# Performance work log

Hardware: AMD Instinct MI355X
Metric: run time of the kernel (lower is better)

The kernel has to match this reference:

```python
import jax, jax.numpy as jnp
import numpy as np

S = 0.7071067811865476  # 1/sqrt(2), pywt haar filter coefficient
# For output j=2k the source coord is k-0.25 (frac 0.75), for j=2k+1 it is k+0.25 (frac 0.25).
_WE = (-0.03515625, 0.26171875, 0.87890625, -0.10546875)  # even outputs, taps at k-2..k+1


def haar_dwt2(x):
    # pywt wavedec2 single level with 'haar': cA=(x0+x1)/sqrt2, cD=(x0-x1)/sqrt2 per pair
    a = (x[..., ::2] + x[..., 1::2]) * S
    d = (x[..., ::2] - x[..., 1::2]) * S
    aa = (a[..., ::2, :] + a[..., 1::2, :]) * S   # LL
    da = (a[..., ::2, :] - a[..., 1::2, :]) * S   # cH (LH)
    ad = (d[..., ::2, :] + d[..., 1::2, :]) * S   # cV (HL)
    dd = (d[..., ::2, :] - d[..., 1::2, :]) * S   # cD (HH)
    return aa, da, ad, dd


def _interleave(e, o, axis):
    stacked = jnp.stack([e, o], axis=axis)
    shp = list(e.shape)
    shp[axis] *= 2
    return stacked.reshape(shp)


def haar_idwt2(aa, da, ad, dd):
    # invert columns (axis -2): x0=(a+d)/sqrt2, x1=(a-d)/sqrt2
    a = _interleave((aa + da) * S, (aa - da) * S, -2)
    d = _interleave((ad + dd) * S, (ad - dd) * S, -2)
    return _interleave((a + d) * S, (a - d) * S, -1)


def area_down2(x):
    h, w = x.shape[-2] // 2, x.shape[-1] // 2
    return x.reshape(*x.shape[:-2], h, 2, w, 2).mean(axis=(-3, -1))


def _up2_last(x):
    n = x.shape[-1]
    p = jnp.pad(x, [(0, 0)] * (x.ndim - 1) + [(2, 2)], mode='edge')  # replicate border like cv2
    ev = (_WE[0] * p[..., 0:n] + _WE[1] * p[..., 1:n + 1]
          + _WE[2] * p[..., 2:n + 2] + _WE[3] * p[..., 3:n + 3])
    od = (_WE[3] * p[..., 1:n + 1] + _WE[2] * p[..., 2:n + 2]
          + _WE[1] * p[..., 3:n + 3] + _WE[0] * p[..., 4:n + 4])
    return jnp.stack([ev, od], axis=-1).reshape(*x.shape[:-1], 2 * n)


def cubic_up2(x):
    x = _up2_last(x)
    return jnp.swapaxes(_up2_last(jnp.swapaxes(x, -1, -2)), -1, -2)


def dwt_roundtrip(x):
    B, C, H, W = x.shape
    # ---- encode ----
    aa1, lh1, hl1, hh1 = haar_dwt2(x)          # level 1: [B,C,H/2,W/2]
    ll2, lh2, hl2, hh2 = haar_dwt2(aa1)        # level 2: [B,C,H/4,W/4]
    bands = jnp.stack([ll2, lh2, hl2, hh2,
                       area_down2(lh1), area_down2(hl1), area_down2(hh1)], axis=2)
    z = bands.reshape(B, C * 7, H // 4, W // 4)
    # ---- decode ----
    b = z.reshape(B, C, 7, H // 4, W // 4)
    lh1u = cubic_up2(b[:, :, 4])
    hl1u = cubic_up2(b[:, :, 5])
    hh1u = cubic_up2(b[:, :, 6])
    aa1r = haar_idwt2(b[:, :, 0], b[:, :, 1], b[:, :, 2], b[:, :, 3])
    return haar_idwt2(aa1r, lh1u, hl1u, hh1u)


def setup_inputs() -> dict:
    key = jax.random.key(0)
    x = jax.random.normal(key, (32, 3, 512, 512), dtype=jnp.float32)
    return {"x": x}


def reference(x):
    return dwt_roundtrip(x)
```

## Files before the change

kernel.cpp:

```cpp
#include <hip/hip_runtime.h>


#define WE0 (-0.03515625f)
#define WE1 (0.26171875f)
#define WE2 (0.87890625f)
#define WE3 (-0.10546875f)

__global__ __launch_bounds__(256) void dwt_encode_kernel(
    const float* __restrict__ x,
    float* __restrict__ aa1,
    float* __restrict__ dlh,
    float* __restrict__ dhl,
    float* __restrict__ dhh)
{
    const int t  = blockIdx.x * 256 + threadIdx.x;
    const int c4 = t & 127;
    const int r4 = (t >> 7) & 127;
    const int bc = t >> 14;

    const float* xp = x + ((size_t)bc << 18);

    float v[4][4];
#pragma unroll
    for (int i = 0; i < 4; ++i) {
        const float4 rv = *reinterpret_cast<const float4*>(
            xp + (size_t)(4 * r4 + i) * 512 + 4 * c4);
        v[i][0] = rv.x; v[i][1] = rv.y; v[i][2] = rv.z; v[i][3] = rv.w;
    }

    float aa[2][2], lhs = 0.f, hls = 0.f, hhs = 0.f;
#pragma unroll
    for (int sr = 0; sr < 2; ++sr) {
#pragma unroll
        for (int sc = 0; sc < 2; ++sc) {
            const float x00 = v[2 * sr][2 * sc],     x01 = v[2 * sr][2 * sc + 1];
            const float x10 = v[2 * sr + 1][2 * sc], x11 = v[2 * sr + 1][2 * sc + 1];
            aa[sr][sc] = 0.5f * (x00 + x01 + x10 + x11);
            lhs += 0.5f * (x00 + x01 - x10 - x11);
            hls += 0.5f * (x00 - x01 + x10 - x11);
            hhs += 0.5f * (x00 - x01 - x10 + x11);
        }
    }

    float* aap = aa1 + ((size_t)bc << 16);
#pragma unroll
    for (int sr = 0; sr < 2; ++sr) {
        *reinterpret_cast<float2*>(aap + (size_t)(2 * r4 + sr) * 256 + 2 * c4) =
            make_float2(aa[sr][0], aa[sr][1]);
    }

    const size_t di = ((size_t)bc << 14) + ((size_t)r4 << 7) + (size_t)c4;
    dlh[di] = 0.25f * lhs;
    dhl[di] = 0.25f * hls;
    dhh[di] = 0.25f * hhs;
}

__global__ __launch_bounds__(256) void dwt_decode_kernel(
    const float* __restrict__ aa1,
    const float* __restrict__ dlh,
    const float* __restrict__ dhl,
    const float* __restrict__ dhh,
    float* __restrict__ out)
{
    const int t  = blockIdx.x * 256 + threadIdx.x;
    const int kc = t & 127;
    const int kr = (t >> 7) & 127;
    const int bc = t >> 14;

    int rs[5], cs[5];
#pragma unroll
    for (int i = 0; i < 5; ++i) {
        rs[i] = min(max(kr - 2 + i, 0), 127);
        cs[i] = min(max(kc - 2 + i, 0), 127);
    }

    const size_t dbase = ((size_t)bc << 14);
    const float* dp[3] = { dlh + dbase, dhl + dbase, dhh + dbase };

    float U[3][2][2];
#pragma unroll
    for (int b = 0; b < 3; ++b) {
        float he[5], ho[5];
#pragma unroll
        for (int i = 0; i < 5; ++i) {
            const float* row = dp[b] + ((size_t)rs[i] << 7);
            const float d0 = row[cs[0]], d1 = row[cs[1]], d2 = row[cs[2]];
            const float d3 = row[cs[3]], d4 = row[cs[4]];
            he[i] = WE0 * d0 + WE1 * d1 + WE2 * d2 + WE3 * d3;
            ho[i] = WE3 * d1 + WE2 * d2 + WE1 * d3 + WE0 * d4;
        }
        U[b][0][0] = WE0 * he[0] + WE1 * he[1] + WE2 * he[2] + WE3 * he[3];
        U[b][0][1] = WE0 * ho[0] + WE1 * ho[1] + WE2 * ho[2] + WE3 * ho[3];
        U[b][1][0] = WE3 * he[1] + WE2 * he[2] + WE1 * he[3] + WE0 * he[4];
        U[b][1][1] = WE3 * ho[1] + WE2 * ho[2] + WE1 * ho[3] + WE0 * ho[4];
    }

    const float* aap = aa1 + ((size_t)bc << 16);
    float* op = out + ((size_t)bc << 18);

#pragma unroll
    for (int i = 0; i < 2; ++i) {
        const float2 aav = *reinterpret_cast<const float2*>(
            aap + (size_t)(2 * kr + i) * 256 + 2 * kc);
        float o0[4], o1[4];
#pragma unroll
        for (int j = 0; j < 2; ++j) {
            const float aaV = (j == 0) ? aav.x : aav.y;
            const float da = U[0][i][j], ad = U[1][i][j], dd = U[2][i][j];
            const float s1 = aaV + da, dd1 = aaV - da;
            const float s2 = ad + dd,  dd2 = ad - dd;
            o0[2 * j]     = 0.5f * (s1 + s2);
            o0[2 * j + 1] = 0.5f * (s1 - s2);
            o1[2 * j]     = 0.5f * (dd1 + dd2);
            o1[2 * j + 1] = 0.5f * (dd1 - dd2);
        }
        *reinterpret_cast<float4*>(op + (size_t)(4 * kr + 2 * i) * 512 + 4 * kc) =
            make_float4(o0[0], o0[1], o0[2], o0[3]);
        *reinterpret_cast<float4*>(op + (size_t)(4 * kr + 2 * i + 1) * 512 + 4 * kc) =
            make_float4(o1[0], o1[1], o1[2], o1[3]);
    }
}

extern "C" void kernel_launch(void* const* d_in, const int* in_sizes, int n_in,
                              void* d_out, int out_size, void* d_ws, size_t ws_size,
                              hipStream_t stream)
{
    const float* x = (const float*)d_in[0];
    float* out = (float*)d_out;
    float* ws  = (float*)d_ws;

    float* aa1 = ws;
    float* dlh = aa1 + (size_t)96 * 256 * 256;
    float* dhl = dlh + (size_t)96 * 128 * 128;
    float* dhh = dhl + (size_t)96 * 128 * 128;

    const int nthreads = 96 * 128 * 128;
    const int blocks   = nthreads / 256;

    dwt_encode_kernel<<<blocks, 256, 0, stream>>>(x, aa1, dlh, dhl, dhh);
    dwt_decode_kernel<<<blocks, 256, 0, stream>>>(aa1, dlh, dhl, dhh, out);
}
```

Baseline: 192.6 us.

## Fuse encode and decode into one tiled kernel with shared-memory halo bands

Replaces the two-kernel pipeline with a single kernel. Each block handles a 128x128 output tile of one image: it recomputes the level-1 detail bands over a 36x36 haloed region, keeps them and the aa1 tile in LDS, then does the cubic upsample and inverse Haar straight from LDS. This removes the global workspace round trip for aa1 and the detail bands, plus one launch. In exchange the halo input is read redundantly (about 27% extra), only 1536 blocks are launched, and per-block LDS use of roughly 32KB may limit occupancy.

```diff
diff --git a/kernel.cpp b/kernel.cpp
--- a/kernel.cpp
+++ b/kernel.cpp
@@ -6,118 +6,114 @@
 #define WE2 (0.87890625f)
 #define WE3 (-0.10546875f)
 
-__global__ __launch_bounds__(256) void dwt_encode_kernel(
-    const float* __restrict__ x,
-    float* __restrict__ aa1,
-    float* __restrict__ dlh,
-    float* __restrict__ dhl,
-    float* __restrict__ dhh)
+__global__ __launch_bounds__(256) void dwt_fused_kernel(
+    const float* __restrict__ x, float* __restrict__ out)
 {
-    const int t  = blockIdx.x * 256 + threadIdx.x;
-    const int c4 = t & 127;
-    const int r4 = (t >> 7) & 127;
-    const int bc = t >> 14;
+    __shared__ float dband[3][36][36];
+    __shared__ float aaT[64][66];
+
+    const int tid  = threadIdx.x;
+    const int b    = blockIdx.x;
+    const int bc   = b >> 4;
+    const int tile = b & 15;
+    const int tr   = tile >> 2;
+    const int tc   = tile & 3;
 
     const float* xp = x + ((size_t)bc << 18);
+    float* op       = out + ((size_t)bc << 18);
 
-    float v[4][4];
+    const int bdr = tr * 32 - 2;
+    const int bdc = tc * 32 - 2;
+
+    for (int task = tid; task < 36 * 36; task += 256) {
+        const int i = task / 36;
+        const int j = task - 36 * i;
+        const int dr = min(max(bdr + i, 0), 127);
+        const int dc = min(max(bdc + j, 0), 127);
+
+        float v[4][4];
 #pragma unroll
-    for (int i = 0; i < 4; ++i) {
-        const float4 rv = *reinterpret_cast<const float4*>(
-            xp + (size_t)(4 * r4 + i) * 512 + 4 * c4);
-        v[i][0] = rv.x; v[i][1] = rv.y; v[i][2] = rv.z; v[i][3] = rv.w;
-    }
+        for (int r = 0; r < 4; ++r) {
+            const float4 rv = *reinterpret_cast<const float4*>(
+                xp + (size_t)(4 * dr + r) * 512 + 4 * dc);
+            v[r][0] = rv.x; v[r][1] = rv.y; v[r][2] = rv.z; v[r][3] = rv.w;
+        }
 
-    float aa[2][2], lhs = 0.f, hls = 0.f, hhs = 0.f;
+        float aa[2][2];
+        float lhs = 0.f, hls = 0.f, hhs = 0.f;
 #pragma unroll
-    for (int sr = 0; sr < 2; ++sr) {
+        for (int sr = 0; sr < 2; ++sr) {
 #pragma unroll
-        for (int sc = 0; sc < 2; ++sc) {
-            const float x00 = v[2 * sr][2 * sc],     x01 = v[2 * sr][2 * sc + 1];
-            const float x10 = v[2 * sr + 1][2 * sc], x11 = v[2 * sr + 1][2 * sc + 1];
-            aa[sr][sc] = 0.5f * (x00 + x01 + x10 + x11);
-            lhs += 0.5f * (x00 + x01 - x10 - x11);
-            hls += 0.5f * (x00 - x01 + x10 - x11);
-            hhs += 0.5f * (x00 - x01 - x10 + x11);
+            for (int sc = 0; sc < 2; ++sc) {
+                const float x00 = v[2*sr][2*sc],   x01 = v[2*sr][2*sc+1];
+                const float x10 = v[2*sr+1][2*sc], x11 = v[2*sr+1][2*sc+1];
+                aa[sr][sc] = 0.5f * (x00 + x01 + x10 + x11);
+                lhs += 0.5f * (x00 + x01 - x10 - x11);
+                hls += 0.5f * (x00 - x01 + x10 - x11);
+                hhs += 0.5f * (x00 - x01 - x10 + x11);
+            }
+        }
+
+        dband[0][i][j] = 0.25f * lhs;
+        dband[1][i][j] = 0.25f * hls;
+        dband[2][i][j] = 0.25f * hhs;
+
+        if ((unsigned)(i - 2) < 32u && (unsigned)(j - 2) < 32u) {
+            const int ar = 2 * (i - 2), ac = 2 * (j - 2);
+            aaT[ar][ac]     = aa[0][0];
+            aaT[ar][ac + 1] = aa[0][1];
+            aaT[ar + 1][ac]     = aa[1][0];
+            aaT[ar + 1][ac + 1] = aa[1][1];
         }
     }
 
-    float* aap = aa1 + ((size_t)bc << 16);
+    __syncthreads();
+
+    for (int blk = tid; blk < 1024; blk += 256) {
+        const int kr = blk >> 5;
+        const int kc = blk & 31;
+
+        float U[3][2][2];
 #pragma unroll
-    for (int sr = 0; sr < 2; ++sr) {
-        *reinterpret_cast<float2*>(aap + (size_t)(2 * r4 + sr) * 256 + 2 * c4) =
-            make_float2(aa[sr][0], aa[sr][1]);
-    }
+        for (int bb = 0; bb < 3; ++bb) {
+            float he[5], ho[5];
+#pragma unroll
+            for (int i = 0; i < 5; ++i) {
+                const float* rowp = &dband[bb][kr + i][kc];
+                const float d0 = rowp[0], d1 = rowp[1], d2 = rowp[2],
+                            d3 = rowp[3], d4 = rowp[4];
+                he[i] = WE0 * d0 + WE1 * d1 + WE2 * d2 + WE3 * d3;
+                ho[i] = WE3 * d1 + WE2 * d2 + WE1 * d3 + WE0 * d4;
+            }
+            U[bb][0][0] = WE0*he[0] + WE1*he[1] + WE2*he[2] + WE3*he[3];
+            U[bb][0][1] = WE0*ho[0] + WE1*ho[1] + WE2*ho[2] + WE3*ho[3];
+            U[bb][1][0] = WE3*he[1] + WE2*he[2] + WE1*he[3] + WE0*he[4];
+            U[bb][1][1] = WE3*ho[1] + WE2*ho[2] + WE1*ho[3] + WE0*ho[4];
+        }
 
-    const size_t di = ((size_t)bc << 14) + ((size_t)r4 << 7) + (size_t)c4;
-    dlh[di] = 0.25f * lhs;
-    dhl[di] = 0.25f * hls;
-    dhh[di] = 0.25f * hhs;
-}
-
-__global__ __launch_bounds__(256) void dwt_decode_kernel(
-    const float* __restrict__ aa1,
-    const float* __restrict__ dlh,
-    const float* __restrict__ dhl,
-    const float* __restrict__ dhh,
-    float* __restrict__ out)
-{
-    const int t  = blockIdx.x * 256 + threadIdx.x;
-    const int kc = t & 127;
-    const int kr = (t >> 7) & 127;
-    const int bc = t >> 14;
-
-    int rs[5], cs[5];
+        const int orow = tr * 128 + 4 * kr;
+        const int ocol = tc * 128 + 4 * kc;
 #pragma unroll
-    for (int i = 0; i < 5; ++i) {
-        rs[i] = min(max(kr - 2 + i, 0), 127);
-        cs[i] = min(max(kc - 2 + i, 0), 127);
-    }
-
-    const size_t dbase = ((size_t)bc << 14);
-    const float* dp[3] = { dlh + dbase, dhl + dbase, dhh + dbase };
-
-    float U[3][2][2];
+        for (int i = 0; i < 2; ++i) {
+            const float a0 = aaT[2*kr + i][2*kc];
+            const float a1 = aaT[2*kr + i][2*kc + 1];
+            float o0[4], o1[4];
 #pragma unroll
-    for (int b = 0; b < 3; ++b) {
-        float he[5], ho[5];
-#pragma unroll
-        for (int i = 0; i < 5; ++i) {
-            const float* row = dp[b] + ((size_t)rs[i] << 7);
-            const float d0 = row[cs[0]], d1 = row[cs[1]], d2 = row[cs[2]];
-            const float d3 = row[cs[3]], d4 = row[cs[4]];
-            he[i] = WE0 * d0 + WE1 * d1 + WE2 * d2 + WE3 * d3;
-            ho[i] = WE3 * d1 + WE2 * d2 + WE1 * d3 + WE0 * d4;
+            for (int j = 0; j < 2; ++j) {
+                const float aaV = (j == 0) ? a0 : a1;
+                const float da = U[0][i][j], ad = U[1][i][j], dd = U[2][i][j];
+                const float s1 = aaV + da, t1 = aaV - da;
+                const float s2 = ad + dd,  t2 = ad - dd;
+                o0[2*j]     = 0.5f * (s1 + s2);
+                o0[2*j + 1] = 0.5f * (s1 - s2);
+                o1[2*j]     = 0.5f * (t1 + t2);
+                o1[2*j + 1] = 0.5f * (t1 - t2);
+            }
+            *reinterpret_cast<float4*>(op + (size_t)(orow + 2*i) * 512 + ocol) =
+                make_float4(o0[0], o0[1], o0[2], o0[3]);
+            *reinterpret_cast<float4*>(op + (size_t)(orow + 2*i + 1) * 512 + ocol) =
+                make_float4(o1[0], o1[1], o1[2], o1[3]);
         }
-        U[b][0][0] = WE0 * he[0] + WE1 * he[1] + WE2 * he[2] + WE3 * he[3];
-        U[b][0][1] = WE0 * ho[0] + WE1 * ho[1] + WE2 * ho[2] + WE3 * ho[3];
-        U[b][1][0] = WE3 * he[1] + WE2 * he[2] + WE1 * he[3] + WE0 * he[4];
-        U[b][1][1] = WE3 * ho[1] + WE2 * ho[2] + WE1 * ho[3] + WE0 * ho[4];
-    }
-
-    const float* aap = aa1 + ((size_t)bc << 16);
-    float* op = out + ((size_t)bc << 18);
-
-#pragma unroll
-    for (int i = 0; i < 2; ++i) {
-        const float2 aav = *reinterpret_cast<const float2*>(
-            aap + (size_t)(2 * kr + i) * 256 + 2 * kc);
-        float o0[4], o1[4];
-#pragma unroll
-        for (int j = 0; j < 2; ++j) {
-            const float aaV = (j == 0) ? aav.x : aav.y;
-            const float da = U[0][i][j], ad = U[1][i][j], dd = U[2][i][j];
-            const float s1 = aaV + da, dd1 = aaV - da;
-            const float s2 = ad + dd,  dd2 = ad - dd;
-            o0[2 * j]     = 0.5f * (s1 + s2);
-            o0[2 * j + 1] = 0.5f * (s1 - s2);
-            o1[2 * j]     = 0.5f * (dd1 + dd2);
-            o1[2 * j + 1] = 0.5f * (dd1 - dd2);
-        }
-        *reinterpret_cast<float4*>(op + (size_t)(4 * kr + 2 * i) * 512 + 4 * kc) =
-            make_float4(o0[0], o0[1], o0[2], o0[3]);
-        *reinterpret_cast<float4*>(op + (size_t)(4 * kr + 2 * i + 1) * 512 + 4 * kc) =
-            make_float4(o1[0], o1[1], o1[2], o1[3]);
     }
 }
 
@@ -127,16 +123,8 @@
 {
     const float* x = (const float*)d_in[0];
     float* out = (float*)d_out;
-    float* ws  = (float*)d_ws;
+    (void)d_ws; (void)ws_size;
 
-    float* aa1 = ws;
-    float* dlh = aa1 + (size_t)96 * 256 * 256;
-    float* dhl = dlh + (size_t)96 * 128 * 128;
-    float* dhh = dhl + (size_t)96 * 128 * 128;
-
-    const int nthreads = 96 * 128 * 128;
-    const int blocks   = nthreads / 256;
-
-    dwt_encode_kernel<<<blocks, 256, 0, stream>>>(x, aa1, dlh, dhl, dhh);
-    dwt_decode_kernel<<<blocks, 256, 0, stream>>>(aa1, dlh, dhl, dhh, out);
+    const int blocks = 96 * 16;
+    dwt_fused_kernel<<<blocks, 256, 0, stream>>>(x, out);
 }
```

Measured after the change: 184.9 us. 4.0% less time.
